# Optimization experiments

Hardware: AMD Instinct MI355X
Metric: run time of the kernel (lower is better)

## Reference

```python
import jax, jax.numpy as jnp
import numpy as np

B, S, DIN, H, DOUT, E, SEL = 8, 2048, 512, 512, 512, 262144, 512
N = B * S


def setup_inputs() -> dict:
    key = jax.random.key(0)
    ks = jax.random.split(key, 20)
    inp = {
        "x": jax.random.normal(ks[0], (B, S, DIN), dtype=jnp.float32),
        "edge_index": jax.random.randint(ks[1], (2, E), 0, N, dtype=jnp.int64),
        "selected_idx": jax.random.randint(ks[2], (B, SEL), 0, S, dtype=jnp.int64),
        "edge_label": jax.random.randint(ks[3], (E,), 0, 8, dtype=jnp.int64),
    }
    k = 4
    for l, fin in enumerate([DIN, H, H]):
        inp[f"conv{l}_w1"] = jax.random.normal(ks[k], (2 * fin, H), dtype=jnp.float32) * 0.02; k += 1
        inp[f"conv{l}_b1"] = jnp.full((H,), 0.01, dtype=jnp.float32)
        inp[f"conv{l}_w2"] = jax.random.normal(ks[k], (H, H), dtype=jnp.float32) * 0.02; k += 1
        inp[f"conv{l}_b2"] = jnp.full((H,), 0.01, dtype=jnp.float32)
    inp["ffn_w1"] = jax.random.normal(ks[k], (H, H), dtype=jnp.float32) * 0.02; k += 1
    inp["ffn_b1"] = jnp.full((H,), 0.01, dtype=jnp.float32)
    inp["ffn_w2"] = jax.random.normal(ks[k], (H, DOUT), dtype=jnp.float32) * 0.02; k += 1
    inp["ffn_b2"] = jnp.full((DOUT,), 0.01, dtype=jnp.float32)
    return inp


def _ffw(x, w1, b1, w2, b2):
    # FeedForward: fc2(act_dropout(relu(fc1(x)))), dropout=0 in eval
    return jax.nn.relu(x @ w1 + b1) @ w2 + b2


def reference(x, edge_index, selected_idx, edge_label,
              conv0_w1, conv0_b1, conv0_w2, conv0_b2,
              conv1_w1, conv1_b1, conv1_w2, conv1_b2,
              conv2_w1, conv2_b1, conv2_w2, conv2_b2,
              ffn_w1, ffn_b1, ffn_w2, ffn_b2):
    b, s, d = x.shape
    n = b * s
    h = x.reshape(n, d)
    src, dst = edge_index[0], edge_index[1]  # PyG: x_j = source, x_i = target
    convs = [(conv0_w1, conv0_b1, conv0_w2, conv0_b2),
             (conv1_w1, conv1_b1, conv1_w2, conv1_b2),
             (conv2_w1, conv2_b1, conv2_w2, conv2_b2)]
    for w1, b1, w2, b2 in convs:
        xi = h[dst]                                   # [E, F]
        xj = h[src]
        ef = jnp.concatenate([xi, xj - xi], axis=1)   # [E, 2F]
        m = _ffw(ef, w1, b1, w2, b2)                  # per-edge MLP [E, H]
        agg = jax.ops.segment_max(m, dst, num_segments=n)
        agg = jnp.where(jnp.isneginf(agg), 0.0, agg)  # empty segments -> 0 (PyG fill)
        h = jax.nn.relu(agg)                          # dropout p acts as identity in eval
    h = _ffw(h, ffn_w1, ffn_b1, ffn_w2, ffn_b2)
    out = h.reshape(b, s, -1)                         # [B, S, DOUT]
    idx = jnp.broadcast_to(selected_idx[:, :, None], (b, selected_idx.shape[1], out.shape[-1]))
    return jnp.take_along_axis(out, idx, axis=1)      # [B, SEL, DOUT]
```

## Files before the change

kernel.cpp:

```cpp
#include <hip/hip_runtime.h>
#include <hip/hip_bf16.h>


#define N_NODES 16384
#define EDGES   262144
#define HDIM    512
#define SEQ     2048

typedef __attribute__((ext_vector_type(8))) short short8;
typedef __attribute__((ext_vector_type(8))) _Float16 half8;
typedef __attribute__((ext_vector_type(2))) _Float16 half2v;
typedef __attribute__((ext_vector_type(4))) float f32x4;

__device__ __forceinline__ void gld16(const void* g, void* l) {
    __builtin_amdgcn_global_load_lds(
        (const __attribute__((address_space(1))) void*)g,
        (__attribute__((address_space(3))) void*)l, 16, 0, 0);
}
__device__ __forceinline__ unsigned short f2b(float f) {
    unsigned int x = __float_as_uint(f);
    return (unsigned short)((x + 0x7fffu + ((x >> 16) & 1u)) >> 16);
}
__device__ __forceinline__ unsigned short f2h(float f) {
    _Float16 h = (_Float16)f;
    return __builtin_bit_cast(unsigned short, h);
}
__device__ __forceinline__ unsigned int zpack_h(unsigned int u, unsigned int v) {
    half2v a = __builtin_bit_cast(half2v, u);
    half2v b = __builtin_bit_cast(half2v, v);
    half2v s = a + b;
    half2v z = {(_Float16)0.f, (_Float16)0.f};
    half2v r = __builtin_elementwise_max(s, z);
    return __builtin_bit_cast(unsigned int, r);
}
__device__ __forceinline__ short8 frag_ld(const short* S, int row, int q) {
    int p = q ^ ((row >> 1) & 3);
    return *(const short8*)(S + row * 32 + p * 8);
}
__device__ __forceinline__ void stage_tile(const short* G, int kc, short* S, int t) {
#pragma unroll
    for (int it = 0; it < 2; ++it) {
        int lin = it * 256 + t;
        int row = lin >> 2, p = lin & 3;
        int q = p ^ ((row >> 1) & 3);
        gld16(G + (size_t)row * HDIM + kc + q * 8, S + lin * 8);
    }
}
__device__ __forceinline__ void mfma_tile_bf16(const short* As, const short* Bs,
                                               int wm, int wn, int l, f32x4 acc[4][4]) {
    short8 a[4], b[4];
#pragma unroll
    for (int mt = 0; mt < 4; ++mt) a[mt] = frag_ld(As, wm + mt * 16 + (l & 15), l >> 4);
#pragma unroll
    for (int nt = 0; nt < 4; ++nt) b[nt] = frag_ld(Bs, wn + nt * 16 + (l & 15), l >> 4);
#pragma unroll
    for (int mt = 0; mt < 4; ++mt)
#pragma unroll
        for (int nt = 0; nt < 4; ++nt)
            acc[mt][nt] = __builtin_amdgcn_mfma_f32_16x16x32_bf16(a[mt], b[nt], acc[mt][nt], 0, 0, 0);
}
__device__ __forceinline__ half8 frag64(const short* S, int row, int q) {
    int p = q ^ ((row >> 1) & 7) ^ (row & 1);
    return *(const half8*)(S + row * 64 + p * 8);
}
__device__ __forceinline__ void stageB32(const short* __restrict__ Wt, int n0, int col0,
                                         short* buf, int t) {
#pragma unroll
    for (int it = 0; it < 4; ++it) {
        int lin = it * 256 + t;
        int row = lin >> 2, s = lin & 3;
        int q = s ^ ((row >> 1) & 3);
        gld16(Wt + (size_t)(n0 + row) * HDIM + col0 + q * 8, buf + lin * 8);
    }
}

__global__ __launch_bounds__(256) void hist_kernel(
    const int* __restrict__ dst, int* __restrict__ hist) {
    int idx = blockIdx.x * 256 + threadIdx.x;
    atomicAdd(&hist[dst[idx]], 1);
}
__global__ __launch_bounds__(256) void scan_kernel(
    const int* __restrict__ hist, int* __restrict__ cursor) {
    __shared__ int part[256];
    const int t = threadIdx.x, base = t * 64;
    int sum = 0;
    for (int i = 0; i < 64; ++i) sum += hist[base + i];
    part[t] = sum;
    __syncthreads();
    int run = 0;
    for (int i = 0; i < t; ++i) run += part[i];
    for (int i = 0; i < 64; ++i) {
        int h = hist[base + i];
        cursor[base + i] = run;
        run += h;
    }
}
__global__ __launch_bounds__(256) void scatter_kernel(
    const int* __restrict__ dst, const int* __restrict__ src,
    int* __restrict__ cursor, int* __restrict__ dstS, int* __restrict__ srcS) {
    int idx = blockIdx.x * 256 + threadIdx.x;
    int d = dst[idx];
    int p = atomicAdd(&cursor[d], 1);
    dstS[p] = d;
    srcS[p] = src[idx];
}

__global__ __launch_bounds__(256) void prep_weights_kernel(
    const float* __restrict__ w1, const float* __restrict__ w2,
    short* __restrict__ WdT, short* __restrict__ w1bT, short* __restrict__ W2T) {
    __shared__ float tile[32][33];
    const int which = blockIdx.z;
    const int k0 = blockIdx.x * 32, n0 = blockIdx.y * 32;
    const int tx = threadIdx.x, ty = threadIdx.y;
#pragma unroll
    for (int i = 0; i < 4; ++i) {
        int k = k0 + ty + i * 8, n = n0 + tx;
        float v;
        if (which == 0)      v = w1[k * 512 + n] - w1[(k + 512) * 512 + n];
        else if (which == 1) v = w1[(k + 512) * 512 + n];
        else                 v = w2[k * 512 + n];
        tile[ty + i * 8][tx] = v;
    }
    __syncthreads();
    short* out = which == 0 ? WdT : (which == 1 ? w1bT : W2T);
#pragma unroll
    for (int i = 0; i < 4; ++i) {
        int n = n0 + ty + i * 8, k = k0 + tx;
        float v = tile[tx][ty + i * 8];
        out[(size_t)n * 512 + k] = (short)(which == 2 ? f2h(v) : f2b(v));
    }
}
__global__ __launch_bounds__(256) void tr_kernel(
    const float* __restrict__ W1, const float* __restrict__ W2,
    short* __restrict__ T1, short* __restrict__ T2) {
    __shared__ float tile[32][33];
    const float* W = blockIdx.z ? W2 : W1;
    short* T = blockIdx.z ? T2 : T1;
    const int k0 = blockIdx.x * 32, n0 = blockIdx.y * 32;
    const int tx = threadIdx.x, ty = threadIdx.y;
#pragma unroll
    for (int i = 0; i < 4; ++i)
        tile[ty + i * 8][tx] = W[(k0 + ty + i * 8) * 512 + n0 + tx];
    __syncthreads();
#pragma unroll
    for (int i = 0; i < 4; ++i)
        T[(size_t)(n0 + ty + i * 8) * 512 + k0 + tx] = (short)f2b(tile[tx][ty + i * 8]);
}
__global__ __launch_bounds__(256) void cvt_bf16_kernel(
    const float* __restrict__ x, short* __restrict__ xb) {
    int idx = blockIdx.x * 256 + threadIdx.x;
    float4 v = ((const float4*)x)[idx];
    uint2 o;
    o.x = (unsigned int)f2b(v.x) | ((unsigned int)f2b(v.y) << 16);
    o.y = (unsigned int)f2b(v.z) | ((unsigned int)f2b(v.w) << 16);
    ((uint2*)xb)[idx] = o;
}

__global__ __launch_bounds__(256) void node_gemm_uv_kernel(
    const short* __restrict__ A, const short* __restrict__ WdT,
    const short* __restrict__ w1bT, const float* __restrict__ b1,
    short* __restrict__ U, short* __restrict__ V) {
    __shared__ short As[128 * 32];
    __shared__ short Bs[128 * 32];
    const int t = threadIdx.x;
    const int by = blockIdx.y;
    const short* Wt = (by < 4) ? WdT : w1bT;
    short* C = (by < 4) ? U : V;
    const float* bias = (by < 4) ? b1 : nullptr;
    const int m0 = blockIdx.x * 128, n0 = (by & 3) * 128;
    const int w = t >> 6, l = t & 63;
    const int wm = (w & 1) * 64, wn = (w >> 1) * 64;
    f32x4 acc[4][4] = {};
    for (int kc = 0; kc < HDIM; kc += 32) {
        stage_tile(A + (size_t)m0 * HDIM, kc, As, t);
        stage_tile(Wt + (size_t)n0 * HDIM, kc, Bs, t);
        __syncthreads();
        mfma_tile_bf16(As, Bs, wm, wn, l, acc);
        __syncthreads();
    }
#pragma unroll
    for (int mt = 0; mt < 4; ++mt) {
        int m = m0 + wm + mt * 16 + (l >> 4) * 4;
#pragma unroll
        for (int nt = 0; nt < 4; ++nt) {
            int n = n0 + wn + nt * 16 + (l & 15);
            float bv = bias ? bias[n] : 0.f;
#pragma unroll
            for (int r = 0; r < 4; ++r)
                C[(size_t)(m + r) * HDIM + n] = (short)f2h(acc[mt][nt][r] + bv);
        }
    }
}

__device__ __forceinline__ unsigned int fkey(float m) {
    unsigned int b = __float_as_uint(m);
    return ((int)b < 0) ? ~b : (b | 0x80000000u);
}
__device__ __forceinline__ void kflush(unsigned int* K, int d, int col, float m) {
    atomicMax(K + (((size_t)d) << 9) + col, fkey(m));
}
__global__ __launch_bounds__(256, 4) void edge_mfma_kernel(
    const short* __restrict__ U, const short* __restrict__ V,
    const short* __restrict__ Wt, const int* __restrict__ srcS,
    const int* __restrict__ dstS, unsigned int* __restrict__ K) {
    __shared__ short As[64 * 64];
    __shared__ short Bs[2][256 * 32];
    const int t = threadIdx.x;
    const int L  = blockIdx.x;
    const int g  = (L >> 4) * 8 + (L & 7);
    const int nh = (L >> 3) & 1;
    const int e0 = g * 64, n0 = nh * 256;
    const int w = t >> 6, l = t & 63;
    const int wnb = w * 64;
    const int lm = l & 15;
    const int arow = t >> 2, s0 = (t & 3) * 2;
    const int perm = ((arow >> 1) & 7) ^ (arow & 1);
    const int p0 = s0 ^ perm, p1 = (s0 + 1) ^ perm;
    const int drow = dstS[e0 + arow];
    const int srow = srcS[e0 + arow];
    const short* up = U + (((size_t)drow) << 9) + s0 * 8;
    const short* vp = V + (((size_t)srow) << 9) + s0 * 8;
    unsigned int* As_u = (unsigned int*)As;
    f32x4 acc[4][4] = {};
    uint4 pu0, pu1, pv0, pv1;
    stageB32(Wt, n0, 0, Bs[0], t);
    pu0 = *(const uint4*)(up);
    pu1 = *(const uint4*)(up + 8);
    pv0 = *(const uint4*)(vp);
    pv1 = *(const uint4*)(vp + 8);
#pragma unroll
    for (int hh = 0; hh < 16; ++hh) {
        const int kc = (hh >> 1) * 64;
        if (hh < 15) {
            const int c1 = ((hh + 1) >> 1) * 64 + ((hh + 1) & 1) * 32;
            stageB32(Wt, n0, c1, Bs[(hh + 1) & 1], t);
        }
        if ((hh & 1) == 0) {
            uint4 z0, z1;
            z0.x = zpack_h(pu0.x, pv0.x); z0.y = zpack_h(pu0.y, pv0.y);
            z0.z = zpack_h(pu0.z, pv0.z); z0.w = zpack_h(pu0.w, pv0.w);
            z1.x = zpack_h(pu1.x, pv1.x); z1.y = zpack_h(pu1.y, pv1.y);
            z1.z = zpack_h(pu1.z, pv1.z); z1.w = zpack_h(pu1.w, pv1.w);
            *(uint4*)(As_u + arow * 32 + p0 * 4) = z0;
            *(uint4*)(As_u + arow * 32 + p1 * 4) = z1;
            if (hh < 14) {
                pu0 = *(const uint4*)(up + kc + 64);
                pu1 = *(const uint4*)(up + kc + 64 + 8);
                pv0 = *(const uint4*)(vp + kc + 64);
                pv1 = *(const uint4*)(vp + kc + 64 + 8);
            }
        }
        if (hh < 14)       asm volatile("s_waitcnt vmcnt(8) lgkmcnt(0)" ::: "memory");
        else if (hh == 14) asm volatile("s_waitcnt vmcnt(4) lgkmcnt(0)" ::: "memory");
        else               asm volatile("s_waitcnt vmcnt(0) lgkmcnt(0)" ::: "memory");
        __builtin_amdgcn_s_barrier();
        asm volatile("" ::: "memory");
        const short* Bb = Bs[hh & 1];
        const int hq = (hh & 1) * 4 + (l >> 4);
        __builtin_amdgcn_s_setprio(1);
        half8 b[4];
#pragma unroll
        for (int nt = 0; nt < 4; ++nt) {
            int row = wnb + nt * 16 + lm;
            int p = (l >> 4) ^ ((row >> 1) & 3);
            b[nt] = *(const half8*)(Bb + row * 32 + p * 8);
        }
#pragma unroll
        for (int mt = 0; mt < 4; ++mt) {
            half8 a = frag64(As, mt * 16 + lm, hq);
#pragma unroll
            for (int nt = 0; nt < 4; ++nt)
                acc[mt][nt] = __builtin_amdgcn_mfma_f32_16x16x32_f16(a, b[nt], acc[mt][nt], 0, 0, 0);
        }
        __builtin_amdgcn_s_setprio(0);
        asm volatile("" ::: "memory");
        __builtin_amdgcn_s_barrier();
    }
    const int dbase = dstS[e0];
    const int drange = dstS[e0 + 63] - dbase + 1;
    unsigned int* tile = (unsigned int*)Bs[1];
    if (drange <= 16) {
        uint4 zz = {0u, 0u, 0u, 0u};
#pragma unroll
        for (int i = 0; i < 4; ++i) ((uint4*)tile)[i * 256 + t] = zz;
        __syncthreads();
#pragma unroll
        for (int mt = 0; mt < 4; ++mt) {
            int base = mt * 16 + (l >> 4) * 4;
            const int4 dd = *(const int4*)(dstS + e0 + base);
            int r0 = dd.x - dbase, r1 = dd.y - dbase, r2 = dd.z - dbase, r3 = dd.w - dbase;
#pragma unroll
            for (int nt = 0; nt < 4; ++nt) {
                int colb = wnb + nt * 16 + lm;
                f32x4 a = acc[mt][nt];
                float m = a[0];
                if (r1 == r0) m = fmaxf(m, a[1]);
                else { atomicMax(tile + r0 * 256 + colb, fkey(m)); m = a[1]; }
                if (r2 == r1) m = fmaxf(m, a[2]);
                else { atomicMax(tile + r1 * 256 + colb, fkey(m)); m = a[2]; }
                if (r3 == r2) m = fmaxf(m, a[3]);
                else { atomicMax(tile + r2 * 256 + colb, fkey(m)); m = a[3]; }
                atomicMax(tile + r3 * 256 + colb, fkey(m));
            }
        }
        __syncthreads();
#pragma unroll 4
        for (int r = 0; r < 16; ++r) {
            if (r < drange) {
                unsigned int kv = tile[r * 256 + t];
                if (kv) {
                    unsigned int* addr = K + (((size_t)(dbase + r)) << 9) + n0 + t;
                    if (r > 0 && r < drange - 1) *addr = kv;
                    else atomicMax(addr, kv);
                }
            }
        }
    } else {
#pragma unroll
        for (int mt = 0; mt < 4; ++mt) {
            int base = mt * 16 + (l >> 4) * 4;
            const int4 dd = *(const int4*)(dstS + e0 + base);
            int d0 = dd.x, d1 = dd.y, d2 = dd.z, d3 = dd.w;
#pragma unroll
            for (int nt = 0; nt < 4; ++nt) {
                int col = n0 + wnb + nt * 16 + lm;
                f32x4 a = acc[mt][nt];
                float m = a[0];
                if (d1 == d0) m = fmaxf(m, a[1]); else { kflush(K, d0, col, m); m = a[1]; }
                if (d2 == d1) m = fmaxf(m, a[2]); else { kflush(K, d1, col, m); m = a[2]; }
                if (d3 == d2) m = fmaxf(m, a[3]); else { kflush(K, d2, col, m); m = a[3]; }
                kflush(K, d3, col, m);
            }
        }
    }
}

__global__ __launch_bounds__(256) void decode_kernel(
    unsigned int* __restrict__ K, const float* __restrict__ b2,
    short* __restrict__ hb) {
    int idx = blockIdx.x * 256 + threadIdx.x;
    unsigned int k = K[idx];
    K[idx] = 0u;
    int c = idx & (HDIM - 1);
    float v = 0.f;
    if (k != 0u) {
        unsigned int b = (k & 0x80000000u) ? (k ^ 0x80000000u) : ~k;
        v = __uint_as_float(b) + b2[c];
    }
    hb[idx] = (short)f2b(fmaxf(v, 0.f));
}

__global__ __launch_bounds__(256) void gather_bf16_kernel(
    const short* __restrict__ hb, const int* __restrict__ sel,
    short* __restrict__ hgb) {
    int idx = blockIdx.x * 256 + threadIdx.x;
    int row = idx >> 6, c = idx & 63;
    int b = row >> 9;
    int s = sel[row];
    ((uint4*)hgb)[idx] = ((const uint4*)(hb + (((size_t)(b * SEQ + s)) << 9)))[c];
}

__global__ __launch_bounds__(256) void ffn_gemm_kernel(
    const short* __restrict__ A, const short* __restrict__ Wt,
    const float* __restrict__ bias, short* __restrict__ Cb,
    float* __restrict__ Cf, int relu) {
    __shared__ short As[128 * 32];
    __shared__ short Bs[128 * 32];
    const int t = threadIdx.x;
    const int m0 = blockIdx.x * 128, n0 = blockIdx.y * 128;
    const int w = t >> 6, l = t & 63;
    const int wm = (w & 1) * 64, wn = (w >> 1) * 64;
    f32x4 acc[4][4] = {};
    for (int kc = 0; kc < HDIM; kc += 32) {
        stage_tile(A + (size_t)m0 * HDIM, kc, As, t);
        stage_tile(Wt + (size_t)n0 * HDIM, kc, Bs, t);
        __syncthreads();
        mfma_tile_bf16(As, Bs, wm, wn, l, acc);
        __syncthreads();
    }
#pragma unroll
    for (int mt = 0; mt < 4; ++mt) {
        int m = m0 + wm + mt * 16 + (l >> 4) * 4;
#pragma unroll
        for (int nt = 0; nt < 4; ++nt) {
            int n = n0 + wn + nt * 16 + (l & 15);
            float bv = bias[n];
#pragma unroll
            for (int r = 0; r < 4; ++r) {
                float v = acc[mt][nt][r] + bv;
                if (relu) v = fmaxf(v, 0.f);
                if (Cf) Cf[(size_t)(m + r) * HDIM + n] = v;
                else    Cb[(size_t)(m + r) * HDIM + n] = (short)f2b(v);
            }
        }
    }
}

extern "C" void kernel_launch(void* const* d_in, const int* in_sizes, int n_in,
                              void* d_out, int out_size, void* d_ws, size_t ws_size,
                              hipStream_t stream) {
    const float* x   = (const float*)d_in[0];
    const int*   ei  = (const int*)d_in[1];
    const int*   sel = (const int*)d_in[2];
    const int*   src = ei;
    const int*   dst = ei + EDGES;
    const float* cw1[3] = {(const float*)d_in[4],  (const float*)d_in[8],  (const float*)d_in[12]};
    const float* cb1[3] = {(const float*)d_in[5],  (const float*)d_in[9],  (const float*)d_in[13]};
    const float* cw2[3] = {(const float*)d_in[6],  (const float*)d_in[10], (const float*)d_in[14]};
    const float* cb2[3] = {(const float*)d_in[7],  (const float*)d_in[11], (const float*)d_in[15]};
    const float* fw1 = (const float*)d_in[16];
    const float* fb1 = (const float*)d_in[17];
    const float* fw2 = (const float*)d_in[18];
    const float* fb2 = (const float*)d_in[19];
    float* out = (float*)d_out;

    const size_t MB = 1024 * 1024;
    char* p = (char*)d_ws;
    unsigned int* keys = (unsigned int*)p;
    short* U    = (short*)(p + 32 * MB);
    short* V    = (short*)(p + 48 * MB);
    short* hb   = (short*)(p + 64 * MB);
    short* WdT  = (short*)(p + 80 * MB);
    short* w1bT = WdT + 512 * 512;
    short* W2T  = w1bT + 512 * 512;
    short* fw1T = W2T + 512 * 512;
    short* fw2T = fw1T + 512 * 512;
    int*   dstS = (int*)(p + 83 * MB);
    int*   srcS = (int*)(p + 84 * MB);
    int*   hist = (int*)(p + 85 * MB);
    int*   curs = hist + N_NODES;
    short* hgb  = (short*)(p + 86 * MB);
    short* t1b  = (short*)(p + 90 * MB);

    (void)hipMemsetAsync(hist, 0, N_NODES * sizeof(int), stream);
    hist_kernel<<<EDGES / 256, 256, 0, stream>>>(dst, hist);
    scan_kernel<<<1, 256, 0, stream>>>(hist, curs);
    scatter_kernel<<<EDGES / 256, 256, 0, stream>>>(dst, src, curs, dstS, srcS);

    cvt_bf16_kernel<<<8192, 256, 0, stream>>>(x, hb);
    tr_kernel<<<dim3(16, 16, 2), dim3(32, 8), 0, stream>>>(fw1, fw2, fw1T, fw2T);
    (void)hipMemsetAsync(keys, 0, 32 * MB, stream);

    for (int l = 0; l < 3; ++l) {
        prep_weights_kernel<<<dim3(16, 16, 3), dim3(32, 8), 0, stream>>>(
            cw1[l], cw2[l], WdT, w1bT, W2T);
        node_gemm_uv_kernel<<<dim3(128, 8), 256, 0, stream>>>(hb, WdT, w1bT, cb1[l], U, V);
        edge_mfma_kernel<<<8192, 256, 0, stream>>>(U, V, W2T, srcS, dstS, keys);
        decode_kernel<<<(N_NODES * HDIM) / 256, 256, 0, stream>>>(keys, cb2[l], hb);
    }

    gather_bf16_kernel<<<(4096 * 64) / 256, 256, 0, stream>>>(hb, sel, hgb);
    ffn_gemm_kernel<<<dim3(32, 4), 256, 0, stream>>>(hgb, fw1T, fb1, t1b, nullptr, 1);
    ffn_gemm_kernel<<<dim3(32, 4), 256, 0, stream>>>(t1b, fw2T, fb2, nullptr, out, 0);
}
```

Baseline: 879.7 us.

## Widen edge MFMA blocks to cover all 512 output columns per edge tile

Each edge-MLP block now uses 512 threads and computes all 512 output columns for its 64 edges instead of splitting the columns across two blocks. The gathered and packed U/V A-tile is built once per edge tile rather than twice, halving the gather traffic and the pack work, and the block-level max-reduction tile covers full rows. The cost is doubled LDS for the B buffers and larger blocks with launch bounds 512,4, which may limit occupancy or force register spills. The wait counts and block-to-tile mapping are adjusted to match.

```diff
diff --git a/kernel.cpp b/kernel.cpp
--- a/kernel.cpp
+++ b/kernel.cpp
@@ -63,14 +63,14 @@
     int p = q ^ ((row >> 1) & 7) ^ (row & 1);
     return *(const half8*)(S + row * 64 + p * 8);
 }
-__device__ __forceinline__ void stageB32(const short* __restrict__ Wt, int n0, int col0,
-                                         short* buf, int t) {
+__device__ __forceinline__ void stageB32w(const short* __restrict__ Wt, int col0,
+                                          short* buf, int t) {
 #pragma unroll
     for (int it = 0; it < 4; ++it) {
-        int lin = it * 256 + t;
+        int lin = it * 512 + t;
         int row = lin >> 2, s = lin & 3;
         int q = s ^ ((row >> 1) & 3);
-        gld16(Wt + (size_t)(n0 + row) * HDIM + col0 + q * 8, buf + lin * 8);
+        gld16(Wt + (size_t)row * HDIM + col0 + q * 8, buf + lin * 8);
     }
 }
 
@@ -199,58 +199,50 @@
 __device__ __forceinline__ void kflush(unsigned int* K, int d, int col, float m) {
     atomicMax(K + (((size_t)d) << 9) + col, fkey(m));
 }
-__global__ __launch_bounds__(256, 4) void edge_mfma_kernel(
+__global__ __launch_bounds__(512, 4) void edge_mfma_kernel(
     const short* __restrict__ U, const short* __restrict__ V,
     const short* __restrict__ Wt, const int* __restrict__ srcS,
     const int* __restrict__ dstS, unsigned int* __restrict__ K) {
     __shared__ short As[64 * 64];
-    __shared__ short Bs[2][256 * 32];
+    __shared__ short Bs[2][512 * 32];
     const int t = threadIdx.x;
     const int L  = blockIdx.x;
-    const int g  = (L >> 4) * 8 + (L & 7);
-    const int nh = (L >> 3) & 1;
-    const int e0 = g * 64, n0 = nh * 256;
+    const int g  = (L & 7) * 512 + (L >> 3);
+    const int e0 = g * 64;
     const int w = t >> 6, l = t & 63;
     const int wnb = w * 64;
     const int lm = l & 15;
-    const int arow = t >> 2, s0 = (t & 3) * 2;
+    const int arow = t >> 3, s0 = t & 7;
     const int perm = ((arow >> 1) & 7) ^ (arow & 1);
-    const int p0 = s0 ^ perm, p1 = (s0 + 1) ^ perm;
+    const int p0 = s0 ^ perm;
     const int drow = dstS[e0 + arow];
     const int srow = srcS[e0 + arow];
     const short* up = U + (((size_t)drow) << 9) + s0 * 8;
     const short* vp = V + (((size_t)srow) << 9) + s0 * 8;
     unsigned int* As_u = (unsigned int*)As;
     f32x4 acc[4][4] = {};
-    uint4 pu0, pu1, pv0, pv1;
-    stageB32(Wt, n0, 0, Bs[0], t);
+    uint4 pu0, pv0;
+    stageB32w(Wt, 0, Bs[0], t);
     pu0 = *(const uint4*)(up);
-    pu1 = *(const uint4*)(up + 8);
     pv0 = *(const uint4*)(vp);
-    pv1 = *(const uint4*)(vp + 8);
 #pragma unroll
     for (int hh = 0; hh < 16; ++hh) {
         const int kc = (hh >> 1) * 64;
         if (hh < 15) {
             const int c1 = ((hh + 1) >> 1) * 64 + ((hh + 1) & 1) * 32;
-            stageB32(Wt, n0, c1, Bs[(hh + 1) & 1], t);
+            stageB32w(Wt, c1, Bs[(hh + 1) & 1], t);
         }
         if ((hh & 1) == 0) {
-            uint4 z0, z1;
+            uint4 z0;
             z0.x = zpack_h(pu0.x, pv0.x); z0.y = zpack_h(pu0.y, pv0.y);
             z0.z = zpack_h(pu0.z, pv0.z); z0.w = zpack_h(pu0.w, pv0.w);
-            z1.x = zpack_h(pu1.x, pv1.x); z1.y = zpack_h(pu1.y, pv1.y);
-            z1.z = zpack_h(pu1.z, pv1.z); z1.w = zpack_h(pu1.w, pv1.w);
             *(uint4*)(As_u + arow * 32 + p0 * 4) = z0;
-            *(uint4*)(As_u + arow * 32 + p1 * 4) = z1;
             if (hh < 14) {
                 pu0 = *(const uint4*)(up + kc + 64);
-                pu1 = *(const uint4*)(up + kc + 64 + 8);
                 pv0 = *(const uint4*)(vp + kc + 64);
-                pv1 = *(const uint4*)(vp + kc + 64 + 8);
             }
         }
-        if (hh < 14)       asm volatile("s_waitcnt vmcnt(8) lgkmcnt(0)" ::: "memory");
+        if (hh < 14)       asm volatile("s_waitcnt vmcnt(6) lgkmcnt(0)" ::: "memory");
         else if (hh == 14) asm volatile("s_waitcnt vmcnt(4) lgkmcnt(0)" ::: "memory");
         else               asm volatile("s_waitcnt vmcnt(0) lgkmcnt(0)" ::: "memory");
         __builtin_amdgcn_s_barrier();
@@ -278,11 +270,11 @@
     }
     const int dbase = dstS[e0];
     const int drange = dstS[e0 + 63] - dbase + 1;
-    unsigned int* tile = (unsigned int*)Bs[1];
+    unsigned int* tile = (unsigned int*)Bs[0];
     if (drange <= 16) {
         uint4 zz = {0u, 0u, 0u, 0u};
 #pragma unroll
-        for (int i = 0; i < 4; ++i) ((uint4*)tile)[i * 256 + t] = zz;
+        for (int i = 0; i < 4; ++i) ((uint4*)tile)[i * 512 + t] = zz;
         __syncthreads();
 #pragma unroll
         for (int mt = 0; mt < 4; ++mt) {
@@ -295,21 +287,21 @@
                 f32x4 a = acc[mt][nt];
                 float m = a[0];
                 if (r1 == r0) m = fmaxf(m, a[1]);
-                else { atomicMax(tile + r0 * 256 + colb, fkey(m)); m = a[1]; }
+                else { atomicMax(tile + r0 * 512 + colb, fkey(m)); m = a[1]; }
                 if (r2 == r1) m = fmaxf(m, a[2]);
-                else { atomicMax(tile + r1 * 256 + colb, fkey(m)); m = a[2]; }
+                else { atomicMax(tile + r1 * 512 + colb, fkey(m)); m = a[2]; }
                 if (r3 == r2) m = fmaxf(m, a[3]);
-                else { atomicMax(tile + r2 * 256 + colb, fkey(m)); m = a[3]; }
-                atomicMax(tile + r3 * 256 + colb, fkey(m));
+                else { atomicMax(tile + r2 * 512 + colb, fkey(m)); m = a[3]; }
+                atomicMax(tile + r3 * 512 + colb, fkey(m));
             }
         }
         __syncthreads();
 #pragma unroll 4
         for (int r = 0; r < 16; ++r) {
             if (r < drange) {
-                unsigned int kv = tile[r * 256 + t];
+                unsigned int kv = tile[r * 512 + t];
                 if (kv) {
-                    unsigned int* addr = K + (((size_t)(dbase + r)) << 9) + n0 + t;
+                    unsigned int* addr = K + (((size_t)(dbase + r)) << 9) + t;
                     if (r > 0 && r < drange - 1) *addr = kv;
                     else atomicMax(addr, kv);
                 }
@@ -323,7 +315,7 @@
             int d0 = dd.x, d1 = dd.y, d2 = dd.z, d3 = dd.w;
 #pragma unroll
             for (int nt = 0; nt < 4; ++nt) {
-                int col = n0 + wnb + nt * 16 + lm;
+                int col = wnb + nt * 16 + lm;
                 f32x4 a = acc[mt][nt];
                 float m = a[0];
                 if (d1 == d0) m = fmaxf(m, a[1]); else { kflush(K, d0, col, m); m = a[1]; }
@@ -445,7 +437,7 @@
         prep_weights_kernel<<<dim3(16, 16, 3), dim3(32, 8), 0, stream>>>(
             cw1[l], cw2[l], WdT, w1bT, W2T);
         node_gemm_uv_kernel<<<dim3(128, 8), 256, 0, stream>>>(hb, WdT, w1bT, cb1[l], U, V);
-        edge_mfma_kernel<<<8192, 256, 0, stream>>>(U, V, W2T, srcS, dstS, keys);
+        edge_mfma_kernel<<<4096, 512, 0, stream>>>(U, V, W2T, srcS, dstS, keys);
         decode_kernel<<<(N_NODES * HDIM) / 256, 256, 0, stream>>>(keys, cb2[l], hb);
     }
 
```

Measured after the change: 870.3 us. Within noise of the previous version (-1.1%).

## Triple-buffer weight tiles and double-buffer A tile to drop per-step barrier

Applied to the files above, without the earlier changes.

Restructures the edge MFMA kernel's K-loop so the weight tiles use a three-stage LDS ring and the gathered edge-feature tile is double-buffered. Each iteration now needs only one barrier instead of two, and the next stages are loaded while the current stage is being computed. The added LDS (about 8 KB for A plus 16 KB for B) lowers the launch-bounds occupancy hint from 4 to 2 blocks per CU, which trades fewer resident waves for more overlap.

```diff
diff --git a/kernel.cpp b/kernel.cpp
--- a/kernel.cpp
+++ b/kernel.cpp
@@ -199,12 +199,12 @@
 __device__ __forceinline__ void kflush(unsigned int* K, int d, int col, float m) {
     atomicMax(K + (((size_t)d) << 9) + col, fkey(m));
 }
-__global__ __launch_bounds__(256, 4) void edge_mfma_kernel(
+__global__ __launch_bounds__(256, 2) void edge_mfma_kernel(
     const short* __restrict__ U, const short* __restrict__ V,
     const short* __restrict__ Wt, const int* __restrict__ srcS,
     const int* __restrict__ dstS, unsigned int* __restrict__ K) {
-    __shared__ short As[64 * 64];
-    __shared__ short Bs[2][256 * 32];
+    __shared__ short As[2][64 * 64];
+    __shared__ short Bs[3][256 * 32];
     const int t = threadIdx.x;
     const int L  = blockIdx.x;
     const int g  = (L >> 4) * 8 + (L & 7);
@@ -220,43 +220,54 @@
     const int srow = srcS[e0 + arow];
     const short* up = U + (((size_t)drow) << 9) + s0 * 8;
     const short* vp = V + (((size_t)srow) << 9) + s0 * 8;
-    unsigned int* As_u = (unsigned int*)As;
     f32x4 acc[4][4] = {};
     uint4 pu0, pu1, pv0, pv1;
-    stageB32(Wt, n0, 0, Bs[0], t);
-    pu0 = *(const uint4*)(up);
-    pu1 = *(const uint4*)(up + 8);
-    pv0 = *(const uint4*)(vp);
-    pv1 = *(const uint4*)(vp + 8);
-#pragma unroll
-    for (int hh = 0; hh < 16; ++hh) {
-        const int kc = (hh >> 1) * 64;
-        if (hh < 15) {
-            const int c1 = ((hh + 1) >> 1) * 64 + ((hh + 1) & 1) * 32;
-            stageB32(Wt, n0, c1, Bs[(hh + 1) & 1], t);
-        }
-        if ((hh & 1) == 0) {
-            uint4 z0, z1;
-            z0.x = zpack_h(pu0.x, pv0.x); z0.y = zpack_h(pu0.y, pv0.y);
-            z0.z = zpack_h(pu0.z, pv0.z); z0.w = zpack_h(pu0.w, pv0.w);
-            z1.x = zpack_h(pu1.x, pv1.x); z1.y = zpack_h(pu1.y, pv1.y);
-            z1.z = zpack_h(pu1.z, pv1.z); z1.w = zpack_h(pu1.w, pv1.w);
-            *(uint4*)(As_u + arow * 32 + p0 * 4) = z0;
-            *(uint4*)(As_u + arow * 32 + p1 * 4) = z1;
-            if (hh < 14) {
-                pu0 = *(const uint4*)(up + kc + 64);
-                pu1 = *(const uint4*)(up + kc + 64 + 8);
-                pv0 = *(const uint4*)(vp + kc + 64);
-                pv1 = *(const uint4*)(vp + kc + 64 + 8);
-            }
-        }
-        if (hh < 14)       asm volatile("s_waitcnt vmcnt(8) lgkmcnt(0)" ::: "memory");
-        else if (hh == 14) asm volatile("s_waitcnt vmcnt(4) lgkmcnt(0)" ::: "memory");
+    pu0 = *(const uint4*)(up);      pu1 = *(const uint4*)(up + 8);
+    pv0 = *(const uint4*)(vp);      pv1 = *(const uint4*)(vp + 8);
+    stageB32(Wt, n0, 0,  Bs[0], t);
+    stageB32(Wt, n0, 32, Bs[1], t);
+    {
+        uint4 z0, z1;
+        z0.x = zpack_h(pu0.x, pv0.x); z0.y = zpack_h(pu0.y, pv0.y);
+        z0.z = zpack_h(pu0.z, pv0.z); z0.w = zpack_h(pu0.w, pv0.w);
+        z1.x = zpack_h(pu1.x, pv1.x); z1.y = zpack_h(pu1.y, pv1.y);
+        z1.z = zpack_h(pu1.z, pv1.z); z1.w = zpack_h(pu1.w, pv1.w);
+        unsigned int* du = (unsigned int*)As[0];
+        *(uint4*)(du + arow * 32 + p0 * 4) = z0;
+        *(uint4*)(du + arow * 32 + p1 * 4) = z1;
+    }
+    pu0 = *(const uint4*)(up + 64); pu1 = *(const uint4*)(up + 64 + 8);
+    pv0 = *(const uint4*)(vp + 64); pv1 = *(const uint4*)(vp + 64 + 8);
+#pragma unroll
+    for (int h = 0; h < 16; ++h) {
+        if (h <= 12)       asm volatile("s_waitcnt vmcnt(8) lgkmcnt(0)" ::: "memory");
+        else if (h <= 14)  asm volatile("s_waitcnt vmcnt(4) lgkmcnt(0)" ::: "memory");
         else               asm volatile("s_waitcnt vmcnt(0) lgkmcnt(0)" ::: "memory");
         __builtin_amdgcn_s_barrier();
         asm volatile("" ::: "memory");
-        const short* Bb = Bs[hh & 1];
-        const int hq = (hh & 1) * 4 + (l >> 4);
+        if (h < 14)
+            stageB32(Wt, n0, (h + 2) * 32, Bs[(h + 2) % 3], t);
+        if ((h & 1) == 0) {
+            const int j = h >> 1;
+            if (j <= 6) {
+                uint4 z0, z1;
+                z0.x = zpack_h(pu0.x, pv0.x); z0.y = zpack_h(pu0.y, pv0.y);
+                z0.z = zpack_h(pu0.z, pv0.z); z0.w = zpack_h(pu0.w, pv0.w);
+                z1.x = zpack_h(pu1.x, pv1.x); z1.y = zpack_h(pu1.y, pv1.y);
+                z1.z = zpack_h(pu1.z, pv1.z); z1.w = zpack_h(pu1.w, pv1.w);
+                unsigned int* du = (unsigned int*)As[(j + 1) & 1];
+                *(uint4*)(du + arow * 32 + p0 * 4) = z0;
+                *(uint4*)(du + arow * 32 + p1 * 4) = z1;
+                if (j <= 5) {
+                    const int kn = (j + 2) * 64;
+                    pu0 = *(const uint4*)(up + kn); pu1 = *(const uint4*)(up + kn + 8);
+                    pv0 = *(const uint4*)(vp + kn); pv1 = *(const uint4*)(vp + kn + 8);
+                }
+            }
+        }
+        const short* Ab = As[(h >> 1) & 1];
+        const short* Bb = Bs[h % 3];
+        const int hq = (h & 1) * 4 + (l >> 4);
         __builtin_amdgcn_s_setprio(1);
         half8 b[4];
 #pragma unroll
@@ -267,18 +278,17 @@
         }
 #pragma unroll
         for (int mt = 0; mt < 4; ++mt) {
-            half8 a = frag64(As, mt * 16 + lm, hq);
+            half8 a = frag64(Ab, mt * 16 + lm, hq);
 #pragma unroll
             for (int nt = 0; nt < 4; ++nt)
                 acc[mt][nt] = __builtin_amdgcn_mfma_f32_16x16x32_f16(a, b[nt], acc[mt][nt], 0, 0, 0);
         }
         __builtin_amdgcn_s_setprio(0);
-        asm volatile("" ::: "memory");
-        __builtin_amdgcn_s_barrier();
-    }
+    }
+    __syncthreads();
     const int dbase = dstS[e0];
     const int drange = dstS[e0 + 63] - dbase + 1;
-    unsigned int* tile = (unsigned int*)Bs[1];
+    unsigned int* tile = (unsigned int*)Bs;
     if (drange <= 16) {
         uint4 zz = {0u, 0u, 0u, 0u};
 #pragma unroll
```

Result: slower. 983.5 us (+11.8%).
